# Performance work log

Hardware: AMD Instinct MI355X
Metric: run time of the kernel (lower is better)

The kernel has to match this reference:

```python
import jax, jax.numpy as jnp
import numpy as np


def _haar_dwt(x):
    # pywt 'haar' dwt2 on even-sized inputs: non-overlapping 2x2 blocks.
    # For block [[a,b],[c,d]]: cA=(a+b+c+d)/2, cH=(a+b-c-d)/2,
    # cV=(a-b+c-d)/2, cD=(a-b-c+d)/2  (pywt dec_hi = [-1/sqrt2, 1/sqrt2]).
    B, C, H, W = x.shape
    xb = x.reshape(B, C, H // 2, 2, W // 2, 2)
    a = xb[:, :, :, 0, :, 0]
    b = xb[:, :, :, 0, :, 1]
    c = xb[:, :, :, 1, :, 0]
    d = xb[:, :, :, 1, :, 1]
    ll = (a + b + c + d) * 0.5
    ch = (a + b - c - d) * 0.5
    cv = (a - b + c - d) * 0.5
    cd = (a - b - c + d) * 0.5
    return ll, ch, cv, cd


def _haar_idwt(ll, ch, cv, cd):
    a = (ll + ch + cv + cd) * 0.5
    b = (ll + ch - cv - cd) * 0.5
    c = (ll - ch + cv - cd) * 0.5
    d = (ll - ch - cv + cd) * 0.5
    B, C, h2, w2 = ll.shape
    top = jnp.stack([a, b], axis=-1)   # [B,C,h2,w2,2]
    bot = jnp.stack([c, d], axis=-1)   # [B,C,h2,w2,2]
    y = jnp.stack([top, bot], axis=-3)  # [B,C,h2,2,w2,2]
    return y.reshape(B, C, 2 * h2, 2 * w2)


def _conv2d(x, w, b, groups=1, pad=1):
    y = jax.lax.conv_general_dilated(
        x, w, window_strides=(1, 1), padding=[(pad, pad), (pad, pad)],
        dimension_numbers=('NCHW', 'OIHW', 'NCHW'), feature_group_count=groups)
    return y + b[None, :, None, None]


def setup_inputs() -> dict:
    key = jax.random.key(0)
    ks = jax.random.split(key, 7)
    B, C, H, W = 8, 64, 256, 256
    C4 = 4 * C
    x = jax.random.normal(ks[0], (B, C, H, W), dtype=jnp.float32)
    dw_w = jax.random.normal(ks[1], (C4, 1, 3, 3), dtype=jnp.float32) / 3.0
    dw_b = jax.random.normal(ks[2], (C4,), dtype=jnp.float32) * 0.01
    pw_w = jax.random.normal(ks[3], (C4, C4, 1, 1), dtype=jnp.float32) / float(np.sqrt(C4))
    pw_b = jax.random.normal(ks[4], (C4,), dtype=jnp.float32) * 0.01
    cv_w = jax.random.normal(ks[5], (C4, C4, 3, 3), dtype=jnp.float32) / float(3.0 * np.sqrt(C4))
    cv_b = jax.random.normal(ks[6], (C4,), dtype=jnp.float32) * 0.01
    return {"x": x, "dw_w": dw_w, "dw_b": dw_b, "pw_w": pw_w,
            "pw_b": pw_b, "cv_w": cv_w, "cv_b": cv_b}


def reference(x, dw_w, dw_b, pw_w, pw_b, cv_w, cv_b):
    B, C, H, W = x.shape  # source math requires H == W (spatial transpose)
    C4 = 4 * C
    ll, ch, cv, cd = _haar_dwt(x)
    # Source stores each subband spatially TRANSPOSED (transpose(2,1,0)).
    sub = jnp.stack([jnp.swapaxes(s, -1, -2) for s in (ll, ch, cv, cd)], axis=2)
    t = sub.reshape(B, C4, H // 2, W // 2)  # channel order c*4 + {LL,cH,cV,cD}
    t = _conv2d(t, dw_w, dw_b, groups=C4, pad=1)  # depthwise 3x3
    t = _conv2d(t, pw_w, pw_b, groups=1, pad=0)   # pointwise 1x1
    t = _conv2d(t, cv_w, cv_b, groups=1, pad=1)   # dense 3x3
    t = jax.nn.gelu(t, approximate=False)         # torch nn.GELU() = exact erf
    t = t.reshape(B, C, 4, H // 2, W // 2)
    # Inverse path un-transposes each subband (transpose(0,2) in source).
    ll2, ch2, cv2, cd2 = [jnp.swapaxes(t[:, :, k], -1, -2) for k in range(4)]
    return _haar_idwt(ll2, ch2, cv2, cd2)
```

## Files before the change

kernel.cpp:

```cpp
#include <hip/hip_runtime.h>
#include <hip/hip_bf16.h>

#define DEVI __device__ __forceinline__

typedef __attribute__((ext_vector_type(8))) short abf8;
typedef __attribute__((ext_vector_type(4))) float f32x4;

DEVI unsigned short f2bf(float f) {
  union { __hip_bfloat16 h; unsigned short u; } cvt;
  cvt.h = __float2bfloat16(f);
  return cvt.u;
}
DEVI float bf2f(unsigned short u) {
  return __uint_as_float(((unsigned)u) << 16);
}
DEVI void async16(const void* g, void* l) {
  __builtin_amdgcn_global_load_lds((__attribute__((address_space(1))) void*)(g),
                                   (__attribute__((address_space(3))) void*)(l), 16, 0, 0);
}

__global__ __launch_bounds__(256) void k0w(const float* __restrict__ cv_w,
                                           const float* __restrict__ pw_w,
                                           const float* __restrict__ pw_b,
                                           unsigned short* __restrict__ cvb,
                                           float* __restrict__ pb3) {
  __shared__ __align__(16) unsigned short As[64 * 32];
  __shared__ __align__(16) unsigned short Bs[64 * 32];
  const int t = threadIdx.x;
  const int wv = t >> 6, ln = t & 63, q = ln >> 4, cl = ln & 15;
  const int dd = blockIdx.x;
  const int oc0 = blockIdx.y * 64, ic0 = blockIdx.z * 64;
  f32x4 acc[4] = {};
  float pacc = 0.0f;
  for (int m0 = 0; m0 < 256; m0 += 32) {
    __syncthreads();
    {
      const int ocr = t >> 2, h = t & 3;
      const float* src = cv_w + ((size_t)(oc0 + ocr) * 256 + m0 + h * 8) * 9 + dd;
      unsigned short* dstp = As + ocr * 32 + h * 8;
      for (int j = 0; j < 8; ++j) dstp[j] = f2bf(src[j * 9]);
    }
    for (int idx = t; idx < 2048; idx += 256) {
      int r = idx >> 6, c = idx & 63;
      Bs[c * 32 + r] = f2bf(pw_w[(size_t)(m0 + r) * 256 + ic0 + c]);
    }
    __syncthreads();
    if (blockIdx.z == 0 && t < 64) {
      for (int mk = 0; mk < 32; ++mk) pacc += bf2f(As[t * 32 + mk]) * pw_b[m0 + mk];
    }
    abf8 a0 = *(const abf8*)(As + (wv * 16 + cl) * 32 + q * 8);
    for (int nt = 0; nt < 4; ++nt) {
      abf8 bf = *(const abf8*)(Bs + (nt * 16 + cl) * 32 + q * 8);
      acc[nt] = __builtin_amdgcn_mfma_f32_16x16x32_bf16(a0, bf, acc[nt], 0, 0, 0);
    }
  }
  if (blockIdx.z == 0 && t < 64) pb3[(size_t)(oc0 + t) * 9 + dd] = pacc;
  for (int r = 0; r < 4; ++r)
    for (int nt = 0; nt < 4; ++nt) {
      int oc = oc0 + wv * 16 + q * 4 + r;
      int ic = ic0 + nt * 16 + cl;
      cvb[((size_t)dd << 16) + oc * 256 + ic] = f2bf(acc[nt][r]);
    }
}

__global__ __launch_bounds__(256) void k0q(const float* __restrict__ pb3,
                                           const float* __restrict__ cv_b,
                                           float* __restrict__ bias9) {
  const int oc = threadIdx.x;
  float p[9];
  for (int i = 0; i < 9; ++i) p[i] = pb3[oc * 9 + i];
  const float cb = cv_b[oc];
  for (int uc = 0; uc < 3; ++uc)
    for (int vc = 0; vc < 3; ++vc) {
      int du0 = (uc == 0) ? 1 : 0, du1 = (uc == 2) ? 1 : 2;
      int dv0 = (vc == 0) ? 1 : 0, dv1 = (vc == 2) ? 1 : 2;
      float s = cb;
      for (int du = du0; du <= du1; ++du)
        for (int dv = dv0; dv <= dv1; ++dv) s += p[du * 3 + dv];
      bias9[(uc * 3 + vc) * 256 + oc] = s;
    }
}

__global__ __launch_bounds__(256) void k1a_dwt(const float* __restrict__ x,
                                               unsigned short* __restrict__ t0) {
  __shared__ __align__(16) float L[64 * 65];
  const int t = threadIdx.x;
  const int u0 = (blockIdx.x & 3) * 32;
  const int v0 = (blockIdx.x >> 2) * 32;
  const int c = blockIdx.y, b = blockIdx.z;
  const float* xp = x + (((size_t)(b * 64 + c)) << 16);
  {
    const int row = t >> 2;
    const float* xr = xp + (size_t)(2 * v0 + row) * 256 + 2 * u0;
    float* Lr = L + row * 65;
    for (int j = 0; j < 4; ++j) {
      int col = ((t & 3) + j * 4) * 4;
      float4 val = *(const float4*)(xr + col);
      Lr[col] = val.x; Lr[col + 1] = val.y; Lr[col + 2] = val.z; Lr[col + 3] = val.w;
    }
  }
  __syncthreads();
  const int vv = t & 31;
  const int us = t >> 5;
  const size_t outc = ((size_t)(b * 256 + c * 4)) << 14;
  for (int pass = 0; pass < 4; ++pass) {
    int uu = us * 4 + pass;
    const float* Lp = L + (2 * vv) * 65 + 2 * uu;
    float a = Lp[0], bb = Lp[1], cc = Lp[65], dd = Lp[66];
    float sll = (a + bb + cc + dd) * 0.5f;
    float sch = (a + bb - cc - dd) * 0.5f;
    float scv = (a - bb + cc - dd) * 0.5f;
    float scd = (a - bb - cc + dd) * 0.5f;
    size_t base = outc + ((u0 + uu) << 7) + (v0 + vv);
    t0[base]         = f2bf(sll);
    t0[base + 16384] = f2bf(sch);
    t0[base + 32768] = f2bf(scv);
    t0[base + 49152] = f2bf(scd);
  }
}

__global__ __launch_bounds__(256) void k1b_dw(const unsigned short* __restrict__ t0,
                                              const float* __restrict__ dww,
                                              const float* __restrict__ dwb,
                                              unsigned short* __restrict__ t1) {
  __shared__ __align__(16) unsigned short S[32 * 181];
  __shared__ __align__(16) unsigned short O[128 * 32];
  const int t = threadIdx.x;
  const int u0 = (blockIdx.x >> 3) * 8;
  const int v0 = (blockIdx.x & 7) * 16;
  const int icB = blockIdx.y * 32;
  const int b = blockIdx.z;
  const unsigned short* t0b = t0 + (((size_t)(b * 256 + icB)) << 14);
  for (int idx = t; idx < 5760; idx += 256) {
    int ic = idx / 180;
    int r = idx - ic * 180;
    int uu = r / 18;
    int vvq = r - uu * 18;
    int gu = u0 + uu - 1, gv = v0 + vvq - 1;
    unsigned short val = 0;
    if ((unsigned)gu < 128u && (unsigned)gv < 128u)
      val = t0b[((size_t)ic << 14) + (gu << 7) + gv];
    S[ic * 181 + r] = val;
  }
  __syncthreads();
  const int icp = t & 15, uu = (t >> 4) & 7, vh = t >> 7;
  const int cc0 = icB + icp * 2;
  float w0[9], w1[9];
  const float* wp = dww + cc0 * 9;
  for (int i = 0; i < 9; ++i) { w0[i] = wp[i]; w1[i] = wp[9 + i]; }
  const float b0 = dwb[cc0], b1 = dwb[cc0 + 1];
  const unsigned short* S0 = S + (icp * 2) * 181 + uu * 18 + vh * 8;
  const unsigned short* S1 = S0 + 181;
  float a0[3][3], a1[3][3];
  for (int du = 0; du < 3; ++du)
    for (int dv = 0; dv < 2; ++dv) {
      a0[du][dv] = bf2f(S0[du * 18 + dv]);
      a1[du][dv] = bf2f(S1[du * 18 + dv]);
    }
  unsigned* O32 = (unsigned*)O;
  for (int vv = 0; vv < 8; ++vv) {
    for (int du = 0; du < 3; ++du) {
      a0[du][2] = bf2f(S0[du * 18 + vv + 2]);
      a1[du][2] = bf2f(S1[du * 18 + vv + 2]);
    }
    float s0 = b0, s1 = b1;
    for (int du = 0; du < 3; ++du)
      for (int dv = 0; dv < 3; ++dv) {
        s0 += w0[du * 3 + dv] * a0[du][dv];
        s1 += w1[du * 3 + dv] * a1[du][dv];
      }
    int p = uu * 16 + vh * 8 + vv;
    O32[p * 16 + icp] = (unsigned)f2bf(s0) | ((unsigned)f2bf(s1) << 16);
    for (int du = 0; du < 3; ++du) {
      a0[du][0] = a0[du][1]; a0[du][1] = a0[du][2];
      a1[du][0] = a1[du][1]; a1[du][1] = a1[du][2];
    }
  }
  __syncthreads();
  const int p = t >> 1, hf = t & 1;
  const int pu = p >> 4, pv = p & 15;
  size_t gp = (size_t)((u0 + pu) * 128 + (v0 + pv));
  const uint4* src = (const uint4*)(O + p * 32 + hf * 16);
  uint4* dst = (uint4*)(t1 + ((((size_t)b * 16384) + gp) << 8) + icB + hf * 16);
  dst[0] = src[0];
  dst[1] = src[1];
}

__global__ __launch_bounds__(256) void k3_cv(const unsigned short* __restrict__ t1,
                                             const unsigned short* __restrict__ cvb,
                                             const float* __restrict__ bias9,
                                             unsigned short* __restrict__ t3) {
  __shared__ __align__(16) char smem[65792];
  unsigned short* As = (unsigned short*)smem;
  unsigned short* Bs = (unsigned short*)(smem + 49152);
  unsigned short* Ost = (unsigned short*)smem;
  const int t = threadIdx.x;
  const int wv = t >> 6, ln = t & 63;
  const int oc0 = blockIdx.x * 128;
  const int u = blockIdx.y;
  const int b = blockIdx.z;
  const unsigned short* t1b = t1 + ((size_t)b << 22);
  const int q = ln >> 4, cl = ln & 15;
  const int lr = ln >> 2, sp = ln & 3;
  const int scA = (sp - (lr >> 1)) & 3;
  const int scB = (sp - ((1 + lr) >> 1)) & 3;
  const int soffA = ((q + (cl >> 1)) & 3) * 8;
  if (t < 64) {
    int pp = t >> 5, r = (t >> 4) & 1, w = t & 15;
    ((unsigned*)Bs)[pp * 2080 + r * 2064 + w] = 0;
  }
  const int du_lo = (u == 0) ? 1 : 0;
  const int NR = (u == 0 || u == 127) ? 16 : 24;

  auto STAGE = [&](int r, int pp) {
    const int du = du_lo + (r >> 3);
    const int ic0 = (r & 7) << 5;
    const int us = u + du - 1;
    const unsigned short* trow = t1b + ((size_t)us << 15);
    const unsigned short* wdu = cvb + (((size_t)(du * 3)) << 16);
    unsigned short* Ap = As + pp * 12288;
    unsigned short* Bp = Bs + pp * 4160;
    for (int g = wv; g < 32; g += 4) {
      if (g < 24) {
        int dv = g >> 3, ch = g & 7;
        async16(wdu + (((size_t)dv) << 16) + (((size_t)(oc0 + ch * 16 + lr)) << 8) + ic0 + scA * 8,
                Ap + dv * 4096 + ch * 512);
      } else {
        int ch = g - 24;
        async16(trow + (((size_t)(ch * 16 + lr)) << 8) + ic0 + scB * 8,
                Bp + 32 + ch * 512);
      }
    }
  };

  f32x4 acc[2][8] = {};
  STAGE(0, 0);
  __syncthreads();
  for (int r = 0; r < NR; ++r) {
    const int pp = r & 1;
    if (r + 1 < NR) STAGE(r + 1, pp ^ 1);
    const unsigned short* Ap = As + pp * 12288;
    const unsigned short* Bp = Bs + pp * 4160;
#pragma unroll
    for (int dv = 0; dv < 3; ++dv) {
      const unsigned short* Adv = Ap + dv * 4096;
      abf8 a0 = *(const abf8*)(Adv + (wv * 32 + cl) * 32 + soffA);
      abf8 a1 = *(const abf8*)(Adv + (wv * 32 + 16 + cl) * 32 + soffA);
      const int slotB = ((q + ((cl + dv) >> 1)) & 3) * 8;
      const unsigned short* Bb = Bp + (cl + dv) * 32 + slotB;
#pragma unroll
      for (int nt = 0; nt < 8; ++nt) {
        abf8 bf = *(const abf8*)(Bb + nt * 512);
        acc[0][nt] = __builtin_amdgcn_mfma_f32_16x16x32_bf16(a0, bf, acc[0][nt], 0, 0, 0);
        acc[1][nt] = __builtin_amdgcn_mfma_f32_16x16x32_bf16(a1, bf, acc[1][nt], 0, 0, 0);
      }
    }
    __syncthreads();
  }
  const int uc = (u == 0) ? 0 : ((u == 127) ? 2 : 1);
  const float* b9 = bias9 + uc * 3 * 256;
  const bool isv0 = (cl == 0), isv127 = (cl == 15);
  for (int mt = 0; mt < 2; ++mt) {
    int ocr = wv * 32 + mt * 16 + q * 4;
    for (int r = 0; r < 4; ++r) {
      int ocA = oc0 + ocr + r;
      float bmid = b9[256 + ocA];
      float blo  = b9[ocA];
      float bhi  = b9[512 + ocA];
      for (int nt = 0; nt < 8; ++nt) {
        float bias = bmid;
        if (nt == 0 && isv0) bias = blo;
        else if (nt == 7 && isv127) bias = bhi;
        float xv = acc[mt][nt][r] + bias;
        float u_ = 0.7978845608028654f * xv * (1.0f + 0.044715f * xv * xv);
        float e = __expf(-2.0f * fabsf(u_));
        float th = (1.0f - e) / (1.0f + e);
        th = (u_ >= 0.0f) ? th : -th;
        float g = 0.5f * xv * (1.0f + th);
        Ost[(ocr + r) * 136 + nt * 16 + cl] = f2bf(g);
      }
    }
  }
  __syncthreads();
  const int rr = t >> 1, hf = t & 1;
  const uint4* src = (const uint4*)(Ost + rr * 136 + hf * 64);
  uint4* dst = (uint4*)(t3 + ((size_t)(b * 256 + oc0 + rr) << 14) + (u << 7) + hf * 64);
  for (int j = 0; j < 8; ++j) dst[j] = src[j];
}

__global__ __launch_bounds__(256) void k4_idwt(const unsigned short* __restrict__ t3,
                                               float* __restrict__ out) {
  __shared__ __align__(16) unsigned short L[4 * 32 * 34];
  const int t = threadIdx.x;
  const int w20 = (blockIdx.x & 3) * 32;
  const int h20 = (blockIdx.x >> 2) * 32;
  const int c = blockIdx.y, b = blockIdx.z;
  const unsigned short* t3b = t3 + (((size_t)(b * 256 + c * 4)) << 14);
  {
    const int row = t >> 1, hf = t & 1;
    const int k = row >> 5, w2i = row & 31;
    const unsigned* g = (const unsigned*)(t3b + ((size_t)k << 14) + ((w20 + w2i) << 7) + h20 + hf * 16);
    unsigned* l = (unsigned*)(L + (k * 32 + w2i) * 34 + hf * 16);
    for (int j = 0; j < 8; ++j) l[j] = g[j];
  }
  __syncthreads();
  const int w2 = t & 31;
  const int h2b = t >> 5;
  float* ob = out + (((size_t)(b * 64 + c)) << 16);
  for (int pass = 0; pass < 4; ++pass) {
    int h2 = h2b + pass * 8;
    int off = w2 * 34 + h2;
    float ll = bf2f(L[off]);
    float ch = bf2f(L[off + 1088]);
    float cv = bf2f(L[off + 2176]);
    float cd = bf2f(L[off + 3264]);
    float A  = (ll + ch + cv + cd) * 0.5f;
    float Bv = (ll + ch - cv - cd) * 0.5f;
    float Cv = (ll - ch + cv - cd) * 0.5f;
    float D  = (ll - ch - cv + cd) * 0.5f;
    int hg = (h20 + h2) * 2, wg = (w20 + w2) * 2;
    *(float2*)(ob + (size_t)hg * 256 + wg)       = make_float2(A, Bv);
    *(float2*)(ob + (size_t)(hg + 1) * 256 + wg) = make_float2(Cv, D);
  }
}

extern "C" void kernel_launch(void* const* d_in, const int* in_sizes, int n_in,
                              void* d_out, int out_size, void* d_ws, size_t ws_size,
                              hipStream_t stream) {
  const float* x    = (const float*)d_in[0];
  const float* dw_w = (const float*)d_in[1];
  const float* dw_b = (const float*)d_in[2];
  const float* pw_w = (const float*)d_in[3];
  const float* pw_b = (const float*)d_in[4];
  const float* cv_w = (const float*)d_in[5];
  const float* cv_b = (const float*)d_in[6];
  char* ws = (char*)d_ws;
  float* pb3           = (float*)ws;
  float* bias9         = (float*)(ws + 16384);
  unsigned short* cvb  = (unsigned short*)(ws + 65536);
  unsigned short* bufA = (unsigned short*)(ws + (size_t)(2u << 20));
  unsigned short* bufB = (unsigned short*)(ws + (size_t)(70u << 20));
  k0w<<<dim3(9, 4, 4), 256, 0, stream>>>(cv_w, pw_w, pw_b, cvb, pb3);
  k0q<<<1, 256, 0, stream>>>(pb3, cv_b, bias9);
  k1a_dwt<<<dim3(16, 64, 8), 256, 0, stream>>>(x, bufA);
  k1b_dw<<<dim3(128, 8, 8), 256, 0, stream>>>(bufA, dw_w, dw_b, bufB);
  k3_cv<<<dim3(2, 128, 8), 256, 0, stream>>>(bufB, cvb, bias9, bufA);
  k4_idwt<<<dim3(16, 64, 8), 256, 0, stream>>>(bufA, (float*)d_out);
}
```

Baseline: 583.2 us.

## Use 2x2 wave tiling and single-buffered LDS in dense 3x3 conv kernel

```diff
diff --git a/kernel.cpp b/kernel.cpp
--- a/kernel.cpp
+++ b/kernel.cpp
@@ -190,12 +190,13 @@
                                              const unsigned short* __restrict__ cvb,
                                              const float* __restrict__ bias9,
                                              unsigned short* __restrict__ t3) {
-  __shared__ __align__(16) char smem[65792];
+  __shared__ __align__(16) char smem[34816];
   unsigned short* As = (unsigned short*)smem;
-  unsigned short* Bs = (unsigned short*)(smem + 49152);
+  unsigned short* Bs = (unsigned short*)(smem + 24576);
   unsigned short* Ost = (unsigned short*)smem;
   const int t = threadIdx.x;
   const int wv = t >> 6, ln = t & 63;
+  const int wm = wv >> 1, wn = wv & 1;
   const int oc0 = blockIdx.x * 128;
   const int u = blockIdx.y;
   const int b = blockIdx.z;
@@ -205,79 +206,69 @@
   const int scA = (sp - (lr >> 1)) & 3;
   const int scB = (sp - ((1 + lr) >> 1)) & 3;
   const int soffA = ((q + (cl >> 1)) & 3) * 8;
-  if (t < 64) {
-    int pp = t >> 5, r = (t >> 4) & 1, w = t & 15;
-    ((unsigned*)Bs)[pp * 2080 + r * 2064 + w] = 0;
-  }
-  const int du_lo = (u == 0) ? 1 : 0;
-  const int NR = (u == 0 || u == 127) ? 16 : 24;
-
-  auto STAGE = [&](int r, int pp) {
-    const int du = du_lo + (r >> 3);
-    const int ic0 = (r & 7) << 5;
+  if (t < 32) ((unsigned*)Bs)[t < 16 ? t : (2064 + (t - 16))] = 0;
+  f32x4 acc[4][4] = {};
+  for (int du = 0; du < 3; ++du) {
     const int us = u + du - 1;
+    if ((unsigned)us >= 128u) continue;
     const unsigned short* trow = t1b + ((size_t)us << 15);
     const unsigned short* wdu = cvb + (((size_t)(du * 3)) << 16);
-    unsigned short* Ap = As + pp * 12288;
-    unsigned short* Bp = Bs + pp * 4160;
-    for (int g = wv; g < 32; g += 4) {
-      if (g < 24) {
-        int dv = g >> 3, ch = g & 7;
-        async16(wdu + (((size_t)dv) << 16) + (((size_t)(oc0 + ch * 16 + lr)) << 8) + ic0 + scA * 8,
-                Ap + dv * 4096 + ch * 512);
-      } else {
-        int ch = g - 24;
-        async16(trow + (((size_t)(ch * 16 + lr)) << 8) + ic0 + scB * 8,
-                Bp + 32 + ch * 512);
+    for (int ic0 = 0; ic0 < 256; ic0 += 32) {
+      __syncthreads();
+      for (int g = wv; g < 32; g += 4) {
+        if (g < 24) {
+          int dv = g >> 3, ch = g & 7;
+          async16(wdu + (((size_t)dv) << 16) + (((size_t)(oc0 + ch * 16 + lr)) << 8) + ic0 + scA * 8,
+                  As + dv * 4096 + ch * 512);
+        } else {
+          int ch = g - 24;
+          async16(trow + (((size_t)(ch * 16 + lr)) << 8) + ic0 + scB * 8,
+                  Bs + 32 + ch * 512);
+        }
       }
-    }
-  };
-
-  f32x4 acc[2][8] = {};
-  STAGE(0, 0);
-  __syncthreads();
-  for (int r = 0; r < NR; ++r) {
-    const int pp = r & 1;
-    if (r + 1 < NR) STAGE(r + 1, pp ^ 1);
-    const unsigned short* Ap = As + pp * 12288;
-    const unsigned short* Bp = Bs + pp * 4160;
+      __syncthreads();
 #pragma unroll
-    for (int dv = 0; dv < 3; ++dv) {
-      const unsigned short* Adv = Ap + dv * 4096;
-      abf8 a0 = *(const abf8*)(Adv + (wv * 32 + cl) * 32 + soffA);
-      abf8 a1 = *(const abf8*)(Adv + (wv * 32 + 16 + cl) * 32 + soffA);
-      const int slotB = ((q + ((cl + dv) >> 1)) & 3) * 8;
-      const unsigned short* Bb = Bp + (cl + dv) * 32 + slotB;
+      for (int dv = 0; dv < 3; ++dv) {
+        const unsigned short* Adv = As + dv * 4096;
+        abf8 a0 = *(const abf8*)(Adv + (wm * 64 + cl) * 32 + soffA);
+        abf8 a1 = *(const abf8*)(Adv + (wm * 64 + 16 + cl) * 32 + soffA);
+        abf8 a2 = *(const abf8*)(Adv + (wm * 64 + 32 + cl) * 32 + soffA);
+        abf8 a3 = *(const abf8*)(Adv + (wm * 64 + 48 + cl) * 32 + soffA);
+        const int slotB = ((q + ((cl + dv) >> 1)) & 3) * 8;
+        const unsigned short* Bb = Bs + (wn * 64 + cl + dv) * 32 + slotB;
 #pragma unroll
-      for (int nt = 0; nt < 8; ++nt) {
-        abf8 bf = *(const abf8*)(Bb + nt * 512);
-        acc[0][nt] = __builtin_amdgcn_mfma_f32_16x16x32_bf16(a0, bf, acc[0][nt], 0, 0, 0);
-        acc[1][nt] = __builtin_amdgcn_mfma_f32_16x16x32_bf16(a1, bf, acc[1][nt], 0, 0, 0);
+        for (int nt = 0; nt < 4; ++nt) {
+          abf8 bf = *(const abf8*)(Bb + nt * 512);
+          acc[0][nt] = __builtin_amdgcn_mfma_f32_16x16x32_bf16(a0, bf, acc[0][nt], 0, 0, 0);
+          acc[1][nt] = __builtin_amdgcn_mfma_f32_16x16x32_bf16(a1, bf, acc[1][nt], 0, 0, 0);
+          acc[2][nt] = __builtin_amdgcn_mfma_f32_16x16x32_bf16(a2, bf, acc[2][nt], 0, 0, 0);
+          acc[3][nt] = __builtin_amdgcn_mfma_f32_16x16x32_bf16(a3, bf, acc[3][nt], 0, 0, 0);
+        }
       }
     }
-    __syncthreads();
-  }
+  }
+  __syncthreads();
   const int uc = (u == 0) ? 0 : ((u == 127) ? 2 : 1);
   const float* b9 = bias9 + uc * 3 * 256;
-  const bool isv0 = (cl == 0), isv127 = (cl == 15);
-  for (int mt = 0; mt < 2; ++mt) {
-    int ocr = wv * 32 + mt * 16 + q * 4;
+  for (int mt = 0; mt < 4; ++mt) {
+    int ocr = wm * 64 + mt * 16 + q * 4;
     for (int r = 0; r < 4; ++r) {
       int ocA = oc0 + ocr + r;
       float bmid = b9[256 + ocA];
       float blo  = b9[ocA];
       float bhi  = b9[512 + ocA];
-      for (int nt = 0; nt < 8; ++nt) {
+      for (int nt = 0; nt < 4; ++nt) {
+        int v = wn * 64 + nt * 16 + cl;
         float bias = bmid;
-        if (nt == 0 && isv0) bias = blo;
-        else if (nt == 7 && isv127) bias = bhi;
+        if (v == 0) bias = blo;
+        else if (v == 127) bias = bhi;
         float xv = acc[mt][nt][r] + bias;
         float u_ = 0.7978845608028654f * xv * (1.0f + 0.044715f * xv * xv);
         float e = __expf(-2.0f * fabsf(u_));
         float th = (1.0f - e) / (1.0f + e);
         th = (u_ >= 0.0f) ? th : -th;
         float g = 0.5f * xv * (1.0f + th);
-        Ost[(ocr + r) * 136 + nt * 16 + cl] = f2bf(g);
+        Ost[(ocr + r) * 136 + v] = f2bf(g);
       }
     }
   }
```

After: 564.2 us. 1.03x faster.
